# Kernel optimization log

Hardware: AMD Instinct MI355X
Metric: run time of the kernel (lower is better)

The kernel has to match this reference:

```python
import jax, jax.numpy as jnp
import numpy as np

PATCH = 3
PAD = (PATCH - 1) // 2
WEIGHT = 100.0
EPS = 1e-9


def _extract_patches(fm):
    # fm: (C, H, W) -> (H*W, C*9) row i*W+j is the reflect-padded 3x3 patch at (i, j)
    C, H, W = fm.shape
    fm_pad = jnp.pad(fm, ((0, 0), (PAD, PAD), (PAD, PAD)), mode='reflect')
    shifts = [fm_pad[:, dh:dh + H, dw:dw + W] for dh in range(PATCH) for dw in range(PATCH)]
    p = jnp.stack(shifts, axis=0)            # (9, C, H, W)
    return p.reshape(PATCH * PATCH * C, H * W).T  # (HW, 9C)


def _match_fm(content_fm, style_fm):
    # content_fm, style_fm: (1, C, H, W); returns matched style fm (1,C,H,W) and idx (2,H,W)
    C, H, W = content_fm.shape[1:]
    cp = _extract_patches(content_fm[0])     # (HW, 9C) content patches (conv kernels)
    sp = _extract_patches(style_fm[0])       # (HW, 9C) style patches (conv sliding windows)
    c_norm = jnp.sqrt(jnp.sum(cp * cp, axis=1))  # kernel_norm per content location
    s_norm = jnp.sqrt(jnp.sum(sp * sp, axis=1))  # style_fm_norm per style location
    score = cp @ sp.T                            # (HW, HW) cross-correlation
    score = score / (c_norm[:, None] * s_norm[None, :] + EPS)
    idx = jnp.argmax(score, axis=1)              # flat argmax == torch.argmax on (H,W) map
    style_flat = style_fm[0].reshape(C, H * W)
    corr = style_flat[:, idx].reshape(1, C, H, W)  # gather matched style pixels
    corr_idx = jnp.stack([idx // W, idx % W], axis=0).reshape(2, H, W)
    return corr, corr_idx


def _masked_gram(fm, mask_flat, mask_sum):
    # fm: (1, C, H, W), mask_flat: (HW,) -> (C, C) gram of masked fm / sum(mask)
    C = fm.shape[1]
    f = fm[0].reshape(C, -1) * mask_flat[None, :]
    return (f @ f.T) / mask_sum


def setup_inputs() -> dict:
    key = jax.random.key(0)
    k1, k2, k3, k4 = jax.random.split(key, 4)
    B, C, H, W = 1, 512, 64, 64
    return {
        'content_fm': jax.random.normal(k1, (B, C, H, W), dtype=jnp.float32),
        'style_fm': jax.random.normal(k2, (B, C, H, W), dtype=jnp.float32),
        'input_fm': jax.random.normal(k3, (B, C, H, W), dtype=jnp.float32),
        'mask': jax.random.uniform(k4, (B, 1, H, W), dtype=jnp.float32),
    }


def reference(content_fm, style_fm, input_fm, mask):
    H, W = content_fm.shape[2:]
    mask_flat = mask[0, 0].reshape(H * W)
    mask_sum = jnp.sum(mask)
    # capture_style_ref: patch-match style fm to content fm, build target gram
    corr_fm, _ = _match_fm(content_fm, style_fm)
    target_gram = _masked_gram(corr_fm, mask_flat, mask_sum)
    # loss mode: masked gram of current image fm vs target, MSE (mean) * weight
    G = _masked_gram(input_fm, mask_flat, mask_sum)
    loss = jnp.mean((G - target_gram) ** 2) * WEIGHT
    return loss
```

## Files before the change

### kernel.cpp

```cpp
#include <hip/hip_runtime.h>

static constexpr int C  = 512;
static constexpr int P  = 4096;

typedef _Float16 half8  __attribute__((ext_vector_type(8)));
typedef float    f32x4  __attribute__((ext_vector_type(4)));

__device__ __forceinline__ int refl(int q) { return q < 0 ? 1 : (q > 63 ? 62 : q); }

__device__ __forceinline__ void g2l16(const void* g, const void* l) {
    __builtin_amdgcn_global_load_lds((const __attribute__((address_space(1))) unsigned int*)g,
                                     (__attribute__((address_space(3))) unsigned int*)l, 16, 0, 0);
}

__global__ __launch_bounds__(256) void k_prep(const float* __restrict__ content, const float* __restrict__ style,
                                              _Float16* __restrict__ Ah, _Float16* __restrict__ Bh,
                                              float* __restrict__ sqn_part, float* __restrict__ msum) {
    __shared__ float T[64][65];
    __shared__ float R4[4][64];
    if (blockIdx.x == 0 && threadIdx.x == 0) msum[0] = 0.f;
    const int p0 = (blockIdx.x & 63) * 64, c0 = (blockIdx.x >> 6) * 64;
    const int pl = threadIdx.x & 63, cq = threadIdx.x >> 6;
    const int pv = threadIdx.x >> 3;
    const int cv = (threadIdx.x & 7) * 8;

    #pragma unroll
    for (int r = 0; r < 16; ++r)
        T[cq + r * 4][pl] = content[(size_t)(c0 + cq + r * 4) * P + p0 + pl];
    __syncthreads();
    #pragma unroll
    for (int r = 0; r < 2; ++r) {
        int pl2 = pv + r * 32;
        half8 v;
        #pragma unroll
        for (int u = 0; u < 8; ++u) v[u] = (_Float16)T[cv + u][pl2];
        *(half8*)(Ah + (size_t)(p0 + pl2) * C + c0 + cv) = v;
    }
    __syncthreads();

    float sq = 0.f;
    #pragma unroll
    for (int r = 0; r < 16; ++r) {
        float v = style[(size_t)(c0 + cq + r * 4) * P + p0 + pl];
        T[cq + r * 4][pl] = v;
        sq += v * v;
    }
    R4[cq][pl] = sq;
    __syncthreads();
    if (cq == 0)
        sqn_part[(size_t)(blockIdx.x >> 6) * P + p0 + pl] = R4[0][pl] + R4[1][pl] + R4[2][pl] + R4[3][pl];
    #pragma unroll
    for (int r = 0; r < 2; ++r) {
        int pl2 = pv + r * 32;
        half8 v;
        #pragma unroll
        for (int u = 0; u < 8; ++u) v[u] = (_Float16)T[cv + u][pl2];
        *(half8*)(Bh + (size_t)(p0 + pl2) * C + c0 + cv) = v;
    }
}

__global__ __launch_bounds__(512, 4) void k_gemm16(const _Float16* __restrict__ Ah,
                                                   const _Float16* __restrict__ Bh,
                                                   float* __restrict__ Eo,
                                                   const float* __restrict__ sqn_part,
                                                   const float* __restrict__ mask,
                                                   float* __restrict__ inv_sn,
                                                   float* __restrict__ msum) {
    __shared__ _Float16 SH[24576];
    const int tid = threadIdx.x;
    const int bid = blockIdx.x;
    const int swz = (bid & 7) * 64 + (bid >> 3);
    const int by = swz >> 4, bx = swz & 15;

    if (bid < 256) {
        float* fsh = (float*)SH;
        const int jw0 = (bid * 16) & 63;
        const int ihh = (bid * 16) >> 6;
        if (tid < 432) {
            const int k = tid & 7, idx = tid >> 3;
            const int t3 = idx / 18, s = idx % 18;
            const int gr = refl(ihh - 1 + t3);
            const int jw = refl(jw0 - 1 + s);
            fsh[tid] = sqn_part[(size_t)k * P + gr * 64 + jw];
        }
        if (tid >= 480 && tid < 496) fsh[432 + tid - 480] = mask[bid * 16 + (tid - 480)];
        __syncthreads();
        if (tid < 54) {
            float s = fsh[tid * 8];
            #pragma unroll
            for (int k = 1; k < 8; ++k) s += fsh[tid * 8 + k];
            fsh[448 + tid] = s;
        }
        __syncthreads();
        if (tid < 16) {
            const float* sq = fsh + 448;
            float s2 = 0.f;
            #pragma unroll
            for (int t3 = 0; t3 < 3; ++t3)
                #pragma unroll
                for (int dd = 0; dd < 3; ++dd)
                    s2 += sq[t3 * 18 + tid + dd];
            inv_sn[bid * 16 + tid] = 1.0f / sqrtf(s2);
        }
        if (tid == 63) {
            float s = fsh[432];
            #pragma unroll
            for (int i = 1; i < 16; ++i) s += fsh[432 + i];
            atomicAdd(msum, s);
        }
        __syncthreads();
    }

    const int wave = tid >> 6, lane = tid & 63;
    const int wr = wave >> 2, wc = wave & 3;
    const int quad = lane >> 4, l15 = lane & 15;
    const int i0 = by * 128, j0 = bx * 256;

    const int r2 = tid >> 2;
    const int gofs = ((tid & 3) ^ (r2 & 3)) * 8;
    const _Float16* pA  = Ah + (size_t)(i0 + r2) * C + gofs;
    const _Float16* pB0 = Bh + (size_t)(j0 + r2) * C + gofs;
    const _Float16* pB1 = pB0 + (size_t)128 * C;
    const int stw = wave * 512;

    const int aslot = (quad ^ (l15 & 3)) * 8;
    int aoff[4], boff[4];
    #pragma unroll
    for (int mi = 0; mi < 4; ++mi) aoff[mi] = (wr * 64 + mi * 16 + l15) * 32 + aslot;
    #pragma unroll
    for (int ni = 0; ni < 4; ++ni) boff[ni] = 4096 + (wc * 64 + ni * 16 + l15) * 32 + aslot;

    f32x4 acc[4][4] = {};
    half8 af[4], bf0, bf1, bf2, bf3;

#define BUF(b) (SH + (b) * 12288)
#define STAGE_A(b,KC) g2l16(pA + (KC), BUF(b) + stw)
#define STAGE_B(b,KC) do { g2l16(pB0 + (KC), BUF(b) + 4096 + stw); \
                           g2l16(pB1 + (KC), BUF(b) + 8192 + stw); } while (0)
#define READ0(b) do { _Pragma("unroll") for (int mi = 0; mi < 4; ++mi) \
                          af[mi] = *(const half8*)(BUF(b) + aoff[mi]); \
                      bf0 = *(const half8*)(BUF(b) + boff[0]); \
                      bf1 = *(const half8*)(BUF(b) + boff[1]); } while (0)
#define READ1(b) do { bf2 = *(const half8*)(BUF(b) + boff[2]); \
                      bf3 = *(const half8*)(BUF(b) + boff[3]); } while (0)
#define MF4(BF,NI) do { _Pragma("unroll") for (int mi = 0; mi < 4; ++mi) \
    acc[mi][NI] = __builtin_amdgcn_mfma_f32_16x16x32_f16(af[mi], BF, acc[mi][NI], 0, 0, 0); } while (0)
#define WAITV0 asm volatile("s_waitcnt vmcnt(0)" ::: "memory")
#define EXEC8(B0,N0,B1,N1) do { \
    __builtin_amdgcn_s_barrier(); \
    asm volatile("s_waitcnt lgkmcnt(0)" ::: "memory"); \
    __builtin_amdgcn_sched_barrier(0); \
    __builtin_amdgcn_s_setprio(1); \
    MF4(B0, N0); MF4(B1, N1); \
    __builtin_amdgcn_s_setprio(0); \
    __builtin_amdgcn_s_barrier(); } while (0)
#define EXEC8W(B0,N0,B1,N1) do { \
    __builtin_amdgcn_s_barrier(); \
    asm volatile("s_waitcnt lgkmcnt(0)" ::: "memory"); \
    __builtin_amdgcn_sched_barrier(0); \
    __builtin_amdgcn_s_setprio(1); \
    MF4(B0, N0); MF4(B1, N1); \
    __builtin_amdgcn_s_setprio(0); \
    WAITV0; \
    __builtin_amdgcn_s_barrier(); } while (0)

    STAGE_A(0, 0); STAGE_B(0, 0);
    WAITV0;
    __builtin_amdgcn_s_barrier();

    #pragma unroll 2
    for (int t = 0; t < 16; ++t) {
        const int b = t & 1;
        const int kn = (t + 1) * 32;
        READ0(b); if (t < 15) STAGE_A(b ^ 1, kn);
        EXEC8(bf0, 0, bf1, 1);
        READ1(b); if (t < 15) STAGE_B(b ^ 1, kn);
        EXEC8W(bf2, 2, bf3, 3);
    }

#undef BUF
#undef STAGE_A
#undef STAGE_B
#undef READ0
#undef READ1
#undef MF4
#undef WAITV0
#undef EXEC8
#undef EXEC8W

    float* SHF = (float*)SH;
    __syncthreads();
    #pragma unroll
    for (int pass = 0; pass < 4; ++pass) {
        const int p = pass >> 1, ch = pass & 1;
        if (wr == p && (wc >> 1) == ch) {
            #pragma unroll
            for (int mi = 0; mi < 4; ++mi) {
                const int row = mi * 16 + quad * 4;
                #pragma unroll
                for (int ni = 0; ni < 4; ++ni) {
                    float* W = SHF + row * 131 + (wc & 1) * 64 + ni * 16 + l15;
                    W[0]   = acc[mi][ni][0];
                    W[131] = acc[mi][ni][1];
                    W[262] = acc[mi][ni][2];
                    W[393] = acc[mi][ni][3];
                }
            }
        }
        __syncthreads();
        {
            const int er  = tid >> 3;
            const int c00 = (tid & 7) * 16;
            const int rm  = (er == 0) ? 1 : er - 1;
            const int rp  = (er == 63) ? 62 : er + 1;
            const float* Rm = SHF + rm * 131;
            const float* Rc = SHF + er * 131;
            const float* Rp = SHF + rp * 131;
            float* outRow = Eo + (size_t)(i0 + p * 64 + er) * P + j0 + ch * 128;
            #pragma unroll
            for (int cc = 0; cc < 16; cc += 8) {
                const int cb  = c00 + cc;
                const int cw0 = cb & 63;
                f32x4 w0, w1;
                #pragma unroll
                for (int u = 0; u < 8; ++u) {
                    int cm = cb - 1 + u, cp = cb + 1 + u;
                    if (u == 0 && cw0 == 0)  cm = cb + 1;
                    if (u == 7 && cw0 == 56) cp = cb + 6;
                    float ev = Rm[cm] + Rc[cb + u] + Rp[cp];
                    if (u < 4) w0[u] = ev; else w1[u - 4] = ev;
                }
                *(f32x4*)(outRow + cb)     = w0;
                *(f32x4*)(outRow + cb + 4) = w1;
            }
        }
        if (pass < 3) __syncthreads();
    }
}

__global__ __launch_bounds__(256) void k_argmax(const float* __restrict__ E,
                                                const float* __restrict__ inv_sn,
                                                int* __restrict__ idxOut) {
    const int i = blockIdx.x;
    const int ih = i >> 6, iw = i & 63;
    const int wave = threadIdx.x >> 6, l = threadIdx.x & 63, l15 = l & 15;
    size_t rb0 = (size_t)(refl(ih - 1) * 64 + iw) * P;
    size_t rb1 = (size_t)(ih * 64 + iw) * P;
    size_t rb2 = (size_t)(refl(ih + 1) * 64 + iw) * P;

    float best = -1e30f;
    int bidx = 0;
    #pragma unroll
    for (int s = 0; s < 4; ++s) {
        const int j0 = (wave * 4 + s) * 256 + l * 4;
        const int jh = j0 >> 6, jw0 = l15 * 4;
        const int cb0 = ((jh == 0) ? 1 : jh - 1) * 64 + jw0;
        const int cb1 = jh * 64 + jw0;
        const int cb2 = ((jh == 63) ? 62 : jh + 1) * 64 + jw0;
        f32x4 u0 = *(const f32x4*)(E + rb0 + cb0);
        f32x4 u1 = *(const f32x4*)(E + rb1 + cb1);
        f32x4 u2 = *(const f32x4*)(E + rb2 + cb2);
        float f0 = u0[0] + u1[0] + u2[0];
        float f1 = u0[1] + u1[1] + u2[1];
        float f2 = u0[2] + u1[2] + u2[2];
        float f3 = u0[3] + u1[3] + u2[3];
        const float4 is = *(const float4*)(inv_sn + j0);
        float v0 = f0 * is.x, v1 = f1 * is.y, v2 = f2 * is.z, v3 = f3 * is.w;
        if (v0 > best) { best = v0; bidx = j0; }
        if (v1 > best) { best = v1; bidx = j0 + 1; }
        if (v2 > best) { best = v2; bidx = j0 + 2; }
        if (v3 > best) { best = v3; bidx = j0 + 3; }
    }

    __shared__ float bv[256];
    __shared__ int   bi[256];
    bv[threadIdx.x] = best;
    bi[threadIdx.x] = bidx;
    __syncthreads();
    for (int t = 128; t > 0; t >>= 1) {
        if (threadIdx.x < t) {
            float ov = bv[threadIdx.x + t];
            int   oi = bi[threadIdx.x + t];
            if (ov > bv[threadIdx.x] || (ov == bv[threadIdx.x] && oi < bi[threadIdx.x])) {
                bv[threadIdx.x] = ov;
                bi[threadIdx.x] = oi;
            }
        }
        __syncthreads();
    }
    if (threadIdx.x == 0) idxOut[i] = bi[0];
}

__global__ __launch_bounds__(256) void k_build(const _Float16* __restrict__ Bh,
                                               const float* __restrict__ input,
                                               const float* __restrict__ mask,
                                               const int* __restrict__ idx,
                                               _Float16* __restrict__ fc, _Float16* __restrict__ fg) {
    __shared__ _Float16 G[16][520];
    __shared__ float mk[16];
    const int p0 = blockIdx.x * 16;
    const int wave = threadIdx.x >> 6, lane = threadIdx.x & 63;

    {
        int e0 = (blockIdx.x * 256 + threadIdx.x) * 32;
        #pragma unroll
        for (int v = 0; v < 4; ++v) {
            int e = e0 + v * 8;
            int pp = e & (P - 1);
            half8 vg;
            #pragma unroll
            for (int u = 0; u < 8; ++u)
                vg[u] = (_Float16)(input[e + u] * mask[pp + u]);
            *(half8*)(fg + e) = vg;
        }
    }

    if (threadIdx.x < 16) mk[threadIdx.x] = mask[p0 + threadIdx.x];

    #pragma unroll
    for (int r = 0; r < 4; ++r) {
        int pp = wave * 4 + r;
        int row = idx[p0 + pp];
        *(half8*)(&G[pp][lane * 8]) = *(const half8*)(Bh + (size_t)row * C + lane * 8);
    }
    __syncthreads();

    #pragma unroll
    for (int h = 0; h < 2; ++h) {
        int c = h * 256 + threadIdx.x;
        half8 o[2];
        #pragma unroll
        for (int q = 0; q < 2; ++q)
            #pragma unroll
            for (int u = 0; u < 8; ++u) {
                int p = q * 8 + u;
                o[q][u] = (_Float16)((float)G[p][c] * mk[p]);
            }
        _Float16* dst = fc + (size_t)c * P + p0;
        *(half8*)(dst)     = o[0];
        *(half8*)(dst + 8) = o[1];
    }
}

__device__ __constant__ int TBX[10] = {0, 0, 1, 0, 1, 2, 0, 1, 2, 3};
__device__ __constant__ int TBY[10] = {0, 1, 1, 2, 2, 2, 3, 3, 3, 3};

__global__ __launch_bounds__(256) void k_gram(const _Float16* __restrict__ fg,
                                              const _Float16* __restrict__ fc,
                                              float* __restrict__ part) {
    const int t = blockIdx.x, z = blockIdx.z;
    const int p0 = z * 256;
    const int wave = threadIdx.x >> 6, lane = threadIdx.x & 63;
    const int wr = wave >> 1, wc = wave & 1, quad = lane >> 4, l15 = lane & 15;
    const int a0 = TBY[t] * 128 + wr * 64, b0 = TBX[t] * 128 + wc * 64;

    f32x4 accg[4][4] = {};
    f32x4 accc[4][4] = {};
    for (int ks = 0; ks < 256; ks += 32) {
        int kbase = p0 + ks + quad * 8;
        half8 af[4], bf[4];
        #pragma unroll
        for (int mi = 0; mi < 4; ++mi) af[mi] = *(const half8*)(fg + (size_t)(a0 + mi * 16 + l15) * P + kbase);
        #pragma unroll
        for (int ni = 0; ni < 4; ++ni) bf[ni] = *(const half8*)(fg + (size_t)(b0 + ni * 16 + l15) * P + kbase);
        #pragma unroll
        for (int mi = 0; mi < 4; ++mi)
            #pragma unroll
            for (int ni = 0; ni < 4; ++ni)
                accg[mi][ni] = __builtin_amdgcn_mfma_f32_16x16x32_f16(af[mi], bf[ni], accg[mi][ni], 0, 0, 0);
        #pragma unroll
        for (int mi = 0; mi < 4; ++mi) af[mi] = *(const half8*)(fc + (size_t)(a0 + mi * 16 + l15) * P + kbase);
        #pragma unroll
        for (int ni = 0; ni < 4; ++ni) bf[ni] = *(const half8*)(fc + (size_t)(b0 + ni * 16 + l15) * P + kbase);
        #pragma unroll
        for (int mi = 0; mi < 4; ++mi)
            #pragma unroll
            for (int ni = 0; ni < 4; ++ni)
                accc[mi][ni] = __builtin_amdgcn_mfma_f32_16x16x32_f16(af[mi], bf[ni], accc[mi][ni], 0, 0, 0);
    }
    float* dst = part + (size_t)(z * 10 + t) * 16384;
    #pragma unroll
    for (int mi = 0; mi < 4; ++mi)
        #pragma unroll
        for (int ni = 0; ni < 4; ++ni)
            #pragma unroll
            for (int r = 0; r < 4; ++r)
                dst[(wr * 64 + mi * 16 + quad * 4 + r) * 128 + wc * 64 + ni * 16 + l15]
                    = accg[mi][ni][r] - accc[mi][ni][r];
}

__global__ void k_loss(const float* __restrict__ part, float* __restrict__ lsum) {
    int e = blockIdx.x * 256 + threadIdx.x;
    int t = e >> 14, loc = e & 16383;
    float d = 0.f;
    #pragma unroll
    for (int z = 0; z < 16; ++z) d += part[(size_t)(z * 10 + t) * 16384 + loc];
    float w = (TBX[t] == TBY[t]) ? 1.0f : 2.0f;
    __shared__ float red[256];
    red[threadIdx.x] = d * d * w;
    __syncthreads();
    for (int s = 128; s > 0; s >>= 1) {
        if (threadIdx.x < s) red[threadIdx.x] += red[threadIdx.x + s];
        __syncthreads();
    }
    if (threadIdx.x == 0) lsum[blockIdx.x] = red[0];
}

__global__ void k_final(const float* __restrict__ lsum, const float* __restrict__ msum,
                        float* __restrict__ out) {
    __shared__ float red[256];
    float s = 0.f;
    for (int e = threadIdx.x; e < 640; e += 256) s += lsum[e];
    red[threadIdx.x] = s;
    __syncthreads();
    for (int t = 128; t > 0; t >>= 1) {
        if (threadIdx.x < t) red[threadIdx.x] += red[threadIdx.x + t];
        __syncthreads();
    }
    if (threadIdx.x == 0) {
        float m = msum[0];
        out[0] = red[0] * 100.0f / (m * m * 262144.0f);
    }
}

extern "C" void kernel_launch(void* const* d_in, const int* in_sizes, int n_in,
                              void* d_out, int out_size, void* d_ws, size_t ws_size,
                              hipStream_t stream) {
    (void)in_sizes; (void)n_in; (void)out_size; (void)ws_size;
    const float* content = (const float*)d_in[0];
    const float* style   = (const float*)d_in[1];
    const float* input   = (const float*)d_in[2];
    const float* mask    = (const float*)d_in[3];

    char* ws = (char*)d_ws;
    float*    Eb   = (float*)ws;
    float*    part = (float*)ws;
    _Float16* Ah   = (_Float16*)(ws + (64u << 20));
    _Float16* Bh   = (_Float16*)(ws + (68u << 20));
    _Float16* fg_h = (_Float16*)(ws + (72u << 20));
    _Float16* fc_h = (_Float16*)(ws + (76u << 20));
    float*    small = (float*)(ws + (80u << 20));
    float* sqn_part = small;
    float* inv_sn   = small + 32768;
    float* msum     = small + 36864;
    float* lsum     = small + 36992;
    int*   idx      = (int*)(small + 37888);
    float* out = (float*)d_out;

    k_prep  <<<512, 256, 0, stream>>>(content, style, Ah, Bh, sqn_part, msum);
    k_gemm16<<<512, 512, 0, stream>>>(Ah, Bh, Eb, sqn_part, mask, inv_sn, msum);
    k_argmax<<<4096, 256, 0, stream>>>(Eb, inv_sn, idx);
    k_build <<<256, 256, 0, stream>>>(Bh, input, mask, idx, fc_h, fg_h);
    k_gram  <<<dim3(10, 1, 16), 256, 0, stream>>>(fg_h, fc_h, part);
    k_loss  <<<640, 256, 0, stream>>>(part, lsum);
    k_final <<<1, 256, 0, stream>>>(lsum, msum, out);
}
```

Measured before the change: 162.0 us.

## Process eight content rows per argmax block with shuffle-based reduction

```diff
diff --git a/kernel.cpp b/kernel.cpp
--- a/kernel.cpp
+++ b/kernel.cpp
@@ -241,54 +241,64 @@
 __global__ __launch_bounds__(256) void k_argmax(const float* __restrict__ E,
                                                 const float* __restrict__ inv_sn,
                                                 int* __restrict__ idxOut) {
-    const int i = blockIdx.x;
-    const int ih = i >> 6, iw = i & 63;
-    const int wave = threadIdx.x >> 6, l = threadIdx.x & 63, l15 = l & 15;
-    size_t rb0 = (size_t)(refl(ih - 1) * 64 + iw) * P;
-    size_t rb1 = (size_t)(ih * 64 + iw) * P;
-    size_t rb2 = (size_t)(refl(ih + 1) * 64 + iw) * P;
-
-    float best = -1e30f;
-    int bidx = 0;
-    #pragma unroll
-    for (int s = 0; s < 4; ++s) {
-        const int j0 = (wave * 4 + s) * 256 + l * 4;
-        const int jh = j0 >> 6, jw0 = l15 * 4;
-        const int cb0 = ((jh == 0) ? 1 : jh - 1) * 64 + jw0;
-        const int cb1 = jh * 64 + jw0;
-        const int cb2 = ((jh == 63) ? 62 : jh + 1) * 64 + jw0;
-        f32x4 u0 = *(const f32x4*)(E + rb0 + cb0);
-        f32x4 u1 = *(const f32x4*)(E + rb1 + cb1);
-        f32x4 u2 = *(const f32x4*)(E + rb2 + cb2);
-        float f0 = u0[0] + u1[0] + u2[0];
-        float f1 = u0[1] + u1[1] + u2[1];
-        float f2 = u0[2] + u1[2] + u2[2];
-        float f3 = u0[3] + u1[3] + u2[3];
-        const float4 is = *(const float4*)(inv_sn + j0);
-        float v0 = f0 * is.x, v1 = f1 * is.y, v2 = f2 * is.z, v3 = f3 * is.w;
-        if (v0 > best) { best = v0; bidx = j0; }
-        if (v1 > best) { best = v1; bidx = j0 + 1; }
-        if (v2 > best) { best = v2; bidx = j0 + 2; }
-        if (v3 > best) { best = v3; bidx = j0 + 3; }
-    }
-
-    __shared__ float bv[256];
-    __shared__ int   bi[256];
-    bv[threadIdx.x] = best;
-    bi[threadIdx.x] = bidx;
-    __syncthreads();
-    for (int t = 128; t > 0; t >>= 1) {
-        if (threadIdx.x < t) {
-            float ov = bv[threadIdx.x + t];
-            int   oi = bi[threadIdx.x + t];
-            if (ov > bv[threadIdx.x] || (ov == bv[threadIdx.x] && oi < bi[threadIdx.x])) {
-                bv[threadIdx.x] = ov;
-                bi[threadIdx.x] = oi;
+    const int tid = threadIdx.x;
+    const int iw = blockIdx.x & 63, g = blockIdx.x >> 6;
+    const int wave = tid >> 6, lane = tid & 63;
+
+    const int jh = tid >> 2, jw0 = (tid & 3) * 16;
+    const int cm = ((jh == 0) ? 1 : jh - 1) * 64 + jw0;
+    const int cc = jh * 64 + jw0;
+    const int cp = ((jh == 63) ? 62 : jh + 1) * 64 + jw0;
+
+    float inv[16];
+    #pragma unroll
+    for (int q4 = 0; q4 < 4; ++q4) {
+        float4 f = *(const float4*)(inv_sn + tid * 16 + q4 * 4);
+        inv[q4 * 4 + 0] = f.x; inv[q4 * 4 + 1] = f.y;
+        inv[q4 * 4 + 2] = f.z; inv[q4 * 4 + 3] = f.w;
+    }
+
+    __shared__ float wbv[8][4];
+    __shared__ int   wbi[8][4];
+
+    #pragma unroll
+    for (int m = 0; m < 8; ++m) {
+        const int ih = g * 8 + m;
+        const size_t rb0 = (size_t)(refl(ih - 1) * 64 + iw) * P;
+        const size_t rb1 = (size_t)(ih * 64 + iw) * P;
+        const size_t rb2 = (size_t)(refl(ih + 1) * 64 + iw) * P;
+        float best = -1e30f;
+        int bidx = 0;
+        #pragma unroll
+        for (int h = 0; h < 4; ++h) {
+            f32x4 u0 = *(const f32x4*)(E + rb0 + cm + h * 4);
+            f32x4 u1 = *(const f32x4*)(E + rb1 + cc + h * 4);
+            f32x4 u2 = *(const f32x4*)(E + rb2 + cp + h * 4);
+            #pragma unroll
+            for (int u = 0; u < 4; ++u) {
+                float v = (u0[u] + u1[u] + u2[u]) * inv[h * 4 + u];
+                int j = tid * 16 + h * 4 + u;
+                if (v > best) { best = v; bidx = j; }
             }
         }
-        __syncthreads();
-    }
-    if (threadIdx.x == 0) idxOut[i] = bi[0];
+        #pragma unroll
+        for (int off = 32; off > 0; off >>= 1) {
+            float ov = __shfl_xor(best, off, 64);
+            int   oi = __shfl_xor(bidx, off, 64);
+            if (ov > best || (ov == best && oi < bidx)) { best = ov; bidx = oi; }
+        }
+        if (lane == 0) { wbv[m][wave] = best; wbi[m][wave] = bidx; }
+    }
+    __syncthreads();
+    if (tid < 8) {
+        float bv = wbv[tid][0]; int bi = wbi[tid][0];
+        #pragma unroll
+        for (int w = 1; w < 4; ++w) {
+            float ov = wbv[tid][w]; int oi = wbi[tid][w];
+            if (ov > bv || (ov == bv && oi < bi)) { bv = ov; bi = oi; }
+        }
+        idxOut[(g * 8 + tid) * 64 + iw] = bi;
+    }
 }
 
 __global__ __launch_bounds__(256) void k_build(const _Float16* __restrict__ Bh,
@@ -449,7 +459,7 @@
 
     k_prep  <<<512, 256, 0, stream>>>(content, style, Ah, Bh, sqn_part, msum);
     k_gemm16<<<512, 512, 0, stream>>>(Ah, Bh, Eb, sqn_part, mask, inv_sn, msum);
-    k_argmax<<<4096, 256, 0, stream>>>(Eb, inv_sn, idx);
+    k_argmax<<<512, 256, 0, stream>>>(Eb, inv_sn, idx);
     k_build <<<256, 256, 0, stream>>>(Bh, input, mask, idx, fc_h, fg_h);
     k_gram  <<<dim3(10, 1, 16), 256, 0, stream>>>(fg_h, fc_h, part);
     k_loss  <<<640, 256, 0, stream>>>(part, lsum);
```

Result: slower. 168.5 us (+4.0%).
